# Kernel tuning notes

Hardware: AMD Instinct MI355X
Metric: run time of the kernel (lower is better)

The kernel has to match this reference:

```python
import math
import jax, jax.numpy as jnp
import numpy as np

D_MODEL = 1024
D_CTX = 1024
NUM_HEADS = 16
ATTN_DIM = 1024
HEAD_DIM = ATTN_DIM // NUM_HEADS  # 64
ROPE_GAMMA = 10.0
ROTARY_BASE = 10000.0
ATTN_SCALE = math.sqrt(ATTN_DIM)  # note: module scales by sqrt(attn_dim), not sqrt(head_dim)


def _apply_rope(x, cos, sin):
    # x: [H,B,T,D]; cos/sin: [1,B,T,D//2]
    half = x.shape[-1] // 2
    x1, x2 = x[..., :half], x[..., half:]
    return jnp.concatenate([x1 * cos - x2 * sin, x1 * sin + x2 * cos], axis=-1)


def setup_inputs() -> dict:
    key = jax.random.key(0)
    ks = jax.random.split(key, 12)
    B, T, L = 4, 1024, 1024
    x = jax.random.normal(ks[0], (B, D_MODEL, T), jnp.float32)
    context = jax.random.normal(ks[1], (B, L, D_CTX), jnp.float32)
    # prefix (padding) masks with per-example valid lengths, as in real padded batches
    lens_q = jnp.array([1024, 896, 768, 640])
    lens_k = jnp.array([1024, 960, 832, 704])
    x_mask = (jnp.arange(T)[None, :] < lens_q[:, None]).astype(jnp.int32)[:, None, :]  # [B,1,T]
    context_mask = (jnp.arange(L)[None, :] < lens_k[:, None]).astype(jnp.int32)[:, None, :]  # [B,1,L]
    s = 0.02
    Wq = jax.random.normal(ks[2], (D_MODEL, ATTN_DIM), jnp.float32) * s
    bq = jax.random.normal(ks[3], (ATTN_DIM,), jnp.float32) * s
    Wk = jax.random.normal(ks[4], (D_CTX, ATTN_DIM), jnp.float32) * s
    bk = jax.random.normal(ks[5], (ATTN_DIM,), jnp.float32) * s
    Wv = jax.random.normal(ks[6], (D_CTX, ATTN_DIM), jnp.float32) * s
    bv = jax.random.normal(ks[7], (ATTN_DIM,), jnp.float32) * s
    Wo = jax.random.normal(ks[8], (ATTN_DIM, D_MODEL), jnp.float32) * s
    bo = jax.random.normal(ks[9], (D_MODEL,), jnp.float32) * s
    return {"x": x, "context": context, "x_mask": x_mask, "context_mask": context_mask,
            "Wq": Wq, "bq": bq, "Wk": Wk, "bk": bk, "Wv": Wv, "bv": bv, "Wo": Wo, "bo": bo}


def reference(x, context, x_mask, context_mask, Wq, bq, Wk, bk, Wv, bv, Wo, bo):
    B, _, T = x.shape
    L = context.shape[1]
    H, D = NUM_HEADS, HEAD_DIM
    xm = x_mask.astype(jnp.float32)          # [B,1,T]
    cmf = context_mask.astype(jnp.float32)   # [B,1,L]

    q = jnp.swapaxes(x, 1, 2) @ Wq + bq      # [B,T,attn_dim]
    k = context @ Wk + bk                    # [B,L,attn_dim]
    v = context @ Wv + bv                    # [B,L,attn_dim]

    q = q.reshape(B, T, H, D).transpose(2, 0, 1, 3)  # [H,B,T,D]
    k = k.reshape(B, L, H, D).transpose(2, 0, 1, 3)  # [H,B,L,D]
    v = v.reshape(B, L, H, D).transpose(2, 0, 1, 3)  # [H,B,L,D]

    # length-normalized RoPE (LARoPE)
    len_q = xm.sum(axis=(-2, -1)).reshape(-1, 1, 1)   # [B,1,1]
    len_k = cmf.sum(axis=(-2, -1)).reshape(-1, 1, 1)  # [B,1,1]
    pos_q = jnp.arange(T, dtype=jnp.float32).reshape(1, -1, 1)
    pos_k = jnp.arange(L, dtype=jnp.float32).reshape(1, -1, 1)
    inv_freq = 1.0 / (ROTARY_BASE ** (jnp.arange(0, D, 2, dtype=jnp.float32) / D))
    theta = (inv_freq * ROPE_GAMMA).reshape(1, 1, -1)  # [1,1,D//2]
    freqs_q = (pos_q / len_q) * theta  # [B,T,D//2]
    freqs_k = (pos_k / len_k) * theta  # [B,L,D//2]
    q = _apply_rope(q, jnp.cos(freqs_q)[None], jnp.sin(freqs_q)[None])
    k = _apply_rope(k, jnp.cos(freqs_k)[None], jnp.sin(freqs_k)[None])

    logits = jnp.einsum('hbtd,hbld->hbtl', q, k) / ATTN_SCALE  # [H,B,T,L]
    key_pad = (context_mask == 0)[None]  # [1,B,1,L]
    logits = jnp.where(key_pad, -jnp.inf, logits)
    attn = jax.nn.softmax(logits, axis=-1)
    query_pad = (x_mask == 0).transpose(1, 0, 2)[..., None]  # [1,B,T,1]
    attn = jnp.where(query_pad, 0.0, attn)

    out = jnp.einsum('hbtl,hbld->hbtd', attn, v)          # [H,B,T,D]
    out = out.transpose(1, 2, 0, 3).reshape(B, T, ATTN_DIM)
    out = out @ Wo + bo                                   # [B,T,d_model]
    out = out * jnp.swapaxes(xm, 1, 2)                    # [B,T,1] broadcast
    return jnp.swapaxes(out, 1, 2)                        # [B,d_model,T]
```

## Files before the change

### kernel.cpp

```cpp
#include <hip/hip_runtime.h>
#include <hip/hip_bf16.h>

typedef __attribute__((ext_vector_type(8))) short s8v;
typedef __attribute__((ext_vector_type(4))) float f4v;
typedef __attribute__((ext_vector_type(4))) unsigned short u4v;
typedef __attribute__((ext_vector_type(2))) unsigned int u2v;

#define NH 16

__device__ __forceinline__ unsigned short f2bf(float f) {
  union { float f; unsigned int u; } v; v.f = f;
  unsigned int r = (v.u + 0x7fffu + ((v.u >> 16) & 1u)) >> 16;
  return (unsigned short)r;
}
__device__ __forceinline__ void gll16(const void* g, void* l) {
  __builtin_amdgcn_global_load_lds((const __attribute__((address_space(1))) void*)g,
                                   (__attribute__((address_space(3))) void*)l, 16, 0, 0);
}
__device__ __forceinline__ unsigned int cvtpk(float lo, float hi) {
  unsigned int r;
  asm volatile("v_cvt_pk_bf16_f32 %0, %1, %2" : "=v"(r) : "v"(lo), "v"(hi));
  return r;
}

__global__ __launch_bounds__(256) void prep_kernel(
    const float* __restrict__ x, const float* __restrict__ ctx,
    const float* __restrict__ Wq, const float* __restrict__ Wk,
    const float* __restrict__ Wv, const float* __restrict__ Wo,
    const int* __restrict__ xm, const int* __restrict__ cm,
    unsigned short* __restrict__ xT, unsigned short* __restrict__ ctxb,
    unsigned short* __restrict__ WqT, unsigned short* __restrict__ WkT,
    unsigned short* __restrict__ WvT, unsigned short* __restrict__ WoT,
    float* __restrict__ lens, float2* __restrict__ rope) {
  const int z = blockIdx.z;
  const int tid = threadIdx.x;
  if (z == 12) {
    if (blockIdx.x | blockIdx.y) return;
    const int w = tid >> 6, lane = tid & 63;
    const int g = w * 2 + (lane >> 5);
    const int l32 = lane & 31;
    const int* m = (g < 4) ? (xm + g * 1024) : (cm + (g - 4) * 1024);
    int s = 0;
    for (int i = l32; i < 1024; i += 32) s += m[i];
    for (int o = 16; o; o >>= 1) s += __shfl_xor(s, o);
    if (l32 == 0) lens[g] = (float)s;
    return;
  }
  if (z == 13) {
    const int idx = blockIdx.y * 32 + blockIdx.x;
    if (idx >= 256) return;
    const int which = idx >> 7;
    const int b = (idx >> 5) & 3;
    const int t0 = (idx & 31) * 32;
    const int* m = (which ? cm : xm) + b * 1024;
    const int lane = tid & 63;
    int s = 0;
    for (int i = lane; i < 1024; i += 64) s += m[i];
    for (int o = 32; o; o >>= 1) s += __shfl_xor(s, o);
    const float len = (float)s;
    const int j = tid & 31;
    const float theta = 10.0f * __expf((float)j * -0.28782313662425572f);
    float2* rt = rope + ((size_t)(which * 4 + b) << 15);
    for (int it = 0; it < 4; ++it) {
      const int t = t0 + (tid >> 5) + it * 8;
      const float fr = (float)t / len * theta;
      float sn, cs;
      __sincosf(fr, &sn, &cs);
      rt[t * 32 + j] = make_float2(cs, sn);
    }
    return;
  }
  if (z >= 8) {
    const float* in = ctx + ((size_t)(z - 8) << 20);
    unsigned short* out = ctxb + ((size_t)(z - 8) << 20);
    const int i = (blockIdx.y * 32 + blockIdx.x) * 1024 + tid * 4;
    const f4v v = *(const f4v*)&in[i];
    u4v o;
#pragma unroll
    for (int j = 0; j < 4; ++j) o[j] = f2bf(v[j]);
    *(u4v*)&out[i] = o;
    return;
  }
  __shared__ unsigned short tile[32][33];
  const float* in;
  unsigned short* out;
  if (z < 4)      { in = x + ((size_t)z << 20); out = xT + ((size_t)z << 20); }
  else if (z == 4){ in = Wq; out = WqT; }
  else if (z == 5){ in = Wk; out = WkT; }
  else if (z == 6){ in = Wv; out = WvT; }
  else            { in = Wo; out = WoT; }
  const int r0 = blockIdx.y * 32, c0 = blockIdx.x * 32;
  const int tx = tid & 31, ty = tid >> 5;
  for (int i = ty; i < 32; i += 8) tile[i][tx] = f2bf(in[(size_t)(r0 + i) * 1024 + c0 + tx]);
  __syncthreads();
  for (int i = ty; i < 32; i += 8) out[(size_t)(c0 + i) * 1024 + r0 + tx] = tile[tx][i];
}

#define STAGE_QKV(buf, kt_) do {                                         \
    const int kn_ = (kt_) * 64;                                          \
    _Pragma("unroll")                                                    \
    for (int i_ = 0; i_ < 4; ++i_) {                                     \
      gll16(Ap + i_ * 32 * 1024 + kn_, &As[buf][(i_ * 256 + tid) * 8]);  \
      gll16(Bp + i_ * 32 * 1024 + kn_, &Bs[buf][(i_ * 256 + tid) * 8]);  \
    }                                                                    \
  } while (0)

__global__ __launch_bounds__(256) void gemm_qkv_kernel(
    const unsigned short* __restrict__ xT, const unsigned short* __restrict__ ctxb,
    const unsigned short* __restrict__ WqT, const unsigned short* __restrict__ WkT,
    const unsigned short* __restrict__ WvT,
    const float* __restrict__ bq, const float* __restrict__ bk, const float* __restrict__ bv,
    unsigned short* __restrict__ Qb, unsigned short* __restrict__ Kb,
    unsigned short* __restrict__ Vtb, const float2* __restrict__ rope) {
  __shared__ __attribute__((aligned(16))) unsigned short As[2][8192];
  __shared__ __attribute__((aligned(16))) unsigned short Bs[2][8192];
  const int id = blockIdx.x + (blockIdx.y << 3) + (blockIdx.z << 8);
  const int rest = id >> 3;
  const int my = (id & 7) + ((rest & 3) << 3);
  const int nx = (rest >> 2) & 7;
  const int mode = rest >> 5;
  const unsigned short* A  = (mode == 0) ? xT : ctxb;
  const unsigned short* Bt = (mode == 0) ? WqT : (mode == 1) ? WkT : WvT;
  const float* bias        = (mode == 0) ? bq : (mode == 1) ? bk : bv;
  const int tid = threadIdx.x;
  const int lane = tid & 63, w = tid >> 6;
  const int lq = lane & 15, lg = lane >> 4;
  const int m0 = my * 128, n0 = nx * 128;
  const int wm = (w & 1) * 64, wn = (w >> 1) * 64;
  const int cswz = (lq & 7) << 3;
  const int srow = tid >> 3;
  const int scol = ((tid & 7) * 8) ^ ((srow & 7) << 3);
  const unsigned short* Ap = A + (size_t)(m0 + srow) * 1024 + scol;
  const unsigned short* Bp = Bt + (size_t)(n0 + srow) * 1024 + scol;
  f4v acc[4][4] = {};

  STAGE_QKV(0, 0);
  STAGE_QKV(1, 1);

  for (int kt = 0; kt < 16; ++kt) {
    const int cur = kt & 1;
    if (kt < 15) {
      asm volatile("s_waitcnt vmcnt(8)" ::: "memory");
    } else {
      asm volatile("s_waitcnt vmcnt(0)" ::: "memory");
    }
    __builtin_amdgcn_s_barrier();
#pragma unroll
    for (int kc = 0; kc < 2; ++kc) {
      s8v af[4], bfr[4];
#pragma unroll
      for (int i = 0; i < 4; ++i)
        af[i] = *(const s8v*)&As[cur][(wm + i * 16 + lq) * 64 + ((kc * 32 + lg * 8) ^ cswz)];
#pragma unroll
      for (int i = 0; i < 4; ++i)
        bfr[i] = *(const s8v*)&Bs[cur][(wn + i * 16 + lq) * 64 + ((kc * 32 + lg * 8) ^ cswz)];
#pragma unroll
      for (int mi = 0; mi < 4; ++mi)
#pragma unroll
        for (int ni = 0; ni < 4; ++ni)
          acc[mi][ni] = __builtin_amdgcn_mfma_f32_16x16x32_bf16(af[mi], bfr[ni], acc[mi][ni], 0, 0, 0);
    }
    __builtin_amdgcn_s_barrier();
    if (kt + 2 < 16) STAGE_QKV(cur, kt + 2);
  }

  float bv4[4];
#pragma unroll
  for (int ni = 0; ni < 4; ++ni) bv4[ni] = bias[n0 + wn + ni * 16 + lq];
  const int b = m0 >> 10;

  if (mode <= 1) {
    unsigned short* O = mode ? Kb : Qb;
    const float2* rt = rope + ((size_t)(mode * 4 + b) << 15);
    const int h = (n0 + wn) >> 6;
#pragma unroll
    for (int mi = 0; mi < 4; ++mi) {
#pragma unroll
      for (int rr = 0; rr < 4; ++rr) {
        const int m = m0 + wm + mi * 16 + lg * 4 + rr;
        const int t = m & 1023;
#pragma unroll
        for (int ni = 0; ni < 2; ++ni) {
          const int jj = ni * 16 + lq;
          const float2 cs2 = rt[t * 32 + jj];
          const float x1 = acc[mi][ni][rr] + bv4[ni];
          const float x2 = acc[mi][ni + 2][rr] + bv4[ni + 2];
          unsigned short* bp = &O[((size_t)((b * NH + h) * 1024 + t)) * 64 + jj];
          bp[0] = f2bf(x1 * cs2.x - x2 * cs2.y);
          bp[32] = f2bf(x1 * cs2.y + x2 * cs2.x);
        }
      }
    }
  } else {
#pragma unroll
    for (int mi = 0; mi < 4; ++mi) {
      const int mbase = m0 + wm + mi * 16 + lg * 4;
      const int l0 = mbase & 1023;
#pragma unroll
      for (int ni = 0; ni < 4; ++ni) {
        const int n = n0 + wn + ni * 16 + lq;
        const int hh = n >> 6, d = n & 63;
        u4v pk;
#pragma unroll
        for (int rr = 0; rr < 4; ++rr) pk[rr] = f2bf(acc[mi][ni][rr] + bv4[ni]);
        *(u4v*)&Vtb[((size_t)((b * NH + hh) * 64 + d)) * 1024 + l0] = pk;
      }
    }
  }
}

__global__ __launch_bounds__(256) void gemm_o_kernel(
    const unsigned short* __restrict__ A, const unsigned short* __restrict__ Bt,
    const float* __restrict__ bias, float* __restrict__ Cout,
    const int* __restrict__ xmask) {
  __shared__ __attribute__((aligned(16))) unsigned short As[2][8192];
  __shared__ __attribute__((aligned(16))) unsigned short Bs[2][8192];
  const int id = blockIdx.x + (blockIdx.y << 3);
  const int rest = id >> 3;
  const int my = (id & 7) + ((rest & 3) << 3);
  const int nx = rest >> 2;
  const int tid = threadIdx.x;
  const int lane = tid & 63, w = tid >> 6;
  const int lq = lane & 15, lg = lane >> 4;
  const int m0 = my * 128, n0 = nx * 128;
  const int wm = (w & 1) * 64, wn = (w >> 1) * 64;
  const int cswz = (lq & 7) << 3;
  const int srow = tid >> 3;
  const int scol = ((tid & 7) * 8) ^ ((srow & 7) << 3);
  const unsigned short* Ap = A + (size_t)(m0 + srow) * 1024 + scol;
  const unsigned short* Bp = Bt + (size_t)(n0 + srow) * 1024 + scol;
  f4v acc[4][4] = {};

  STAGE_QKV(0, 0);
  STAGE_QKV(1, 1);

  for (int kt = 0; kt < 16; ++kt) {
    const int cur = kt & 1;
    if (kt < 15) {
      asm volatile("s_waitcnt vmcnt(8)" ::: "memory");
    } else {
      asm volatile("s_waitcnt vmcnt(0)" ::: "memory");
    }
    __builtin_amdgcn_s_barrier();
#pragma unroll
    for (int kc = 0; kc < 2; ++kc) {
      s8v af[4], bfr[4];
#pragma unroll
      for (int i = 0; i < 4; ++i)
        af[i] = *(const s8v*)&As[cur][(wm + i * 16 + lq) * 64 + ((kc * 32 + lg * 8) ^ cswz)];
#pragma unroll
      for (int i = 0; i < 4; ++i)
        bfr[i] = *(const s8v*)&Bs[cur][(wn + i * 16 + lq) * 64 + ((kc * 32 + lg * 8) ^ cswz)];
#pragma unroll
      for (int mi = 0; mi < 4; ++mi)
#pragma unroll
        for (int ni = 0; ni < 4; ++ni)
          acc[mi][ni] = __builtin_amdgcn_mfma_f32_16x16x32_bf16(af[mi], bfr[ni], acc[mi][ni], 0, 0, 0);
    }
    __builtin_amdgcn_s_barrier();
    if (kt + 2 < 16) STAGE_QKV(cur, kt + 2);
  }

  float bv4[4];
#pragma unroll
  for (int ni = 0; ni < 4; ++ni) bv4[ni] = bias[n0 + wn + ni * 16 + lq];
  const int b = m0 >> 10;
#pragma unroll
  for (int mi = 0; mi < 4; ++mi) {
    const int mbase = m0 + wm + mi * 16 + lg * 4;
    const int t0 = mbase & 1023;
#pragma unroll
    for (int ni = 0; ni < 4; ++ni) {
      const int n = n0 + wn + ni * 16 + lq;
      f4v pk;
#pragma unroll
      for (int rr = 0; rr < 4; ++rr) {
        float v = acc[mi][ni][rr] + bv4[ni];
        v *= (float)xmask[b * 1024 + t0 + rr];
        pk[rr] = v;
      }
      *(f4v*)&Cout[(size_t)b * 1024 * 1024 + (size_t)n * 1024 + t0] = pk;
    }
  }
}

__global__ __launch_bounds__(512) void attn_kernel(
    const unsigned short* __restrict__ Q, const unsigned short* __restrict__ K,
    const unsigned short* __restrict__ Vt, const float* __restrict__ lens,
    unsigned short* __restrict__ Aout) {
  __shared__ __attribute__((aligned(16))) unsigned short Ks[2][4096];
  __shared__ __attribute__((aligned(16))) unsigned short Vs[2][4096];
  __shared__ __attribute__((aligned(16))) unsigned short Plds[8][16][72];
  const int tid = threadIdx.x;
  const int lane = tid & 63, w = tid >> 6;
  const int lq = lane & 15, lg = lane >> 4;
  const int id = blockIdx.x + (blockIdx.y << 3);
  const int bh = (id & 7) + (((id >> 3) & 7) << 3);
  const int qblk = id >> 6;
  const int b = bh >> 4, h = bh & 15;
  const int lenq = (int)lens[b];
  if (qblk * 128 >= lenq) return;
  const int lenk = (int)lens[4 + b];
  const int nkt = (lenk + 63) >> 6;
  const int qrow = qblk * 128 + w * 16;
  const unsigned short* Qp = Q + ((size_t)bh * 1024 + qrow) * 64;
  const unsigned short* Kp = K + (size_t)bh * 65536;
  const unsigned short* Vp = Vt + (size_t)bh * 65536;
  const s8v qf0 = *(const s8v*)&Qp[lq * 64 + lg * 8];
  const s8v qf1 = *(const s8v*)&Qp[lq * 64 + 32 + lg * 8];
  const int r0 = tid >> 3;
  const int c0x = ((tid & 7) * 8) ^ ((r0 & 7) << 3);
  const int cswz = (lq & 7) << 3;

  gll16(&Kp[(size_t)r0 * 64 + c0x], &Ks[0][tid * 8]);
  gll16(&Vp[(size_t)r0 * 1024 + c0x], &Vs[0][tid * 8]);
  __syncthreads();

  const float SC2 = 0.0450842200277f;
  float m_run = -1e30f, s_run = 0.0f;
  f4v ot[4] = {};
  for (int kt = 0; kt < nkt; ++kt) {
    const int p = kt & 1;
    if (kt + 1 < nkt) {
      const int kn = (kt + 1) * 64;
      gll16(&Kp[(size_t)(kn + r0) * 64 + c0x], &Ks[p ^ 1][tid * 8]);
      gll16(&Vp[(size_t)r0 * 1024 + kn + c0x], &Vs[p ^ 1][tid * 8]);
    }
    const int k0 = kt * 64;
    const bool full = (k0 + 64 <= lenk);
    float pvv[16];
    float tmax = -1e30f;
    __builtin_amdgcn_s_setprio(1);
#pragma unroll
    for (int kk = 0; kk < 4; ++kk) {
      const int krow = kk * 16 + lq;
      const s8v a0 = *(const s8v*)&Ks[p][krow * 64 + ((lg * 8) ^ cswz)];
      const s8v a1 = *(const s8v*)&Ks[p][krow * 64 + ((32 + lg * 8) ^ cswz)];
      f4v s = {};
      s = __builtin_amdgcn_mfma_f32_16x16x32_bf16(a0, qf0, s, 0, 0, 0);
      s = __builtin_amdgcn_mfma_f32_16x16x32_bf16(a1, qf1, s, 0, 0, 0);
#pragma unroll
      for (int rr = 0; rr < 4; ++rr) {
        float v = s[rr] * SC2;
        if (!full) {
          const int key = k0 + kk * 16 + lg * 4 + rr;
          if (key >= lenk) v = -1e30f;
        }
        pvv[kk * 4 + rr] = v;
        tmax = fmaxf(tmax, v);
      }
    }
    __builtin_amdgcn_s_setprio(0);
    tmax = fmaxf(tmax, __shfl_xor(tmax, 16));
    tmax = fmaxf(tmax, __shfl_xor(tmax, 32));
    if (__any(tmax > m_run + 8.0f)) {
      const float m_new = fmaxf(m_run, tmax);
      const float alpha = exp2f(m_run - m_new);
#pragma unroll
      for (int d = 0; d < 4; ++d)
#pragma unroll
        for (int j = 0; j < 4; ++j) ot[d][j] *= alpha;
      s_run *= alpha;
      m_run = m_new;
    }
    float psum = 0.0f;
#pragma unroll
    for (int kk = 0; kk < 4; ++kk) {
      const float e0 = exp2f(pvv[kk * 4 + 0] - m_run);
      const float e1 = exp2f(pvv[kk * 4 + 1] - m_run);
      const float e2 = exp2f(pvv[kk * 4 + 2] - m_run);
      const float e3 = exp2f(pvv[kk * 4 + 3] - m_run);
      psum += (e0 + e1) + (e2 + e3);
      u2v pw;
      pw[0] = cvtpk(e0, e1);
      pw[1] = cvtpk(e2, e3);
      *(u2v*)&Plds[w][lq][kk * 16 + lg * 4] = pw;
    }
    psum += __shfl_xor(psum, 16);
    psum += __shfl_xor(psum, 32);
    s_run += psum;
    const s8v pb0 = *(const s8v*)&Plds[w][lq][lg * 8];
    const s8v pb1 = *(const s8v*)&Plds[w][lq][32 + lg * 8];
    __builtin_amdgcn_s_setprio(1);
#pragma unroll
    for (int d = 0; d < 4; ++d) {
      const int vrow = d * 16 + lq;
      const s8v av0 = *(const s8v*)&Vs[p][vrow * 64 + ((lg * 8) ^ cswz)];
      const s8v av1 = *(const s8v*)&Vs[p][vrow * 64 + ((32 + lg * 8) ^ cswz)];
      ot[d] = __builtin_amdgcn_mfma_f32_16x16x32_bf16(av0, pb0, ot[d], 0, 0, 0);
      ot[d] = __builtin_amdgcn_mfma_f32_16x16x32_bf16(av1, pb1, ot[d], 0, 0, 0);
    }
    __builtin_amdgcn_s_setprio(0);
    if (kt + 1 < nkt) __syncthreads();
  }
  const float inv = 1.0f / s_run;
  const int t = qrow + lq;
  unsigned short* op = Aout + ((size_t)(b * 1024 + t)) * 1024 + h * 64;
#pragma unroll
  for (int d = 0; d < 4; ++d) {
    u4v oo;
#pragma unroll
    for (int rr = 0; rr < 4; ++rr) oo[rr] = f2bf(ot[d][rr] * inv);
    *(u4v*)&op[d * 16 + lg * 4] = oo;
  }
}

extern "C" void kernel_launch(void* const* d_in, const int* in_sizes, int n_in,
                              void* d_out, int out_size, void* d_ws, size_t ws_size,
                              hipStream_t stream) {
  const float* x   = (const float*)d_in[0];
  const float* ctx = (const float*)d_in[1];
  const int* xm = (const int*)d_in[2];
  const int* cm = (const int*)d_in[3];
  const float* Wq = (const float*)d_in[4];
  const float* bq = (const float*)d_in[5];
  const float* Wk = (const float*)d_in[6];
  const float* bk = (const float*)d_in[7];
  const float* Wv = (const float*)d_in[8];
  const float* bv = (const float*)d_in[9];
  const float* Wo = (const float*)d_in[10];
  const float* bo = (const float*)d_in[11];

  char* ws = (char*)d_ws;
  const size_t MB = 1024 * 1024;
  unsigned short* xT   = (unsigned short*)(ws);
  unsigned short* AOb  = (unsigned short*)(ws);
  unsigned short* ctxb = (unsigned short*)(ws + 8 * MB);
  unsigned short* WqT  = (unsigned short*)(ws + 16 * MB);
  unsigned short* WkT  = (unsigned short*)(ws + 18 * MB);
  unsigned short* WvT  = (unsigned short*)(ws + 20 * MB);
  unsigned short* WoT  = (unsigned short*)(ws + 22 * MB);
  unsigned short* Qb   = (unsigned short*)(ws + 24 * MB);
  unsigned short* Kb   = (unsigned short*)(ws + 32 * MB);
  unsigned short* Vtb  = (unsigned short*)(ws + 40 * MB);
  float* lens          = (float*)(ws + 48 * MB);
  float2* rope         = (float2*)(ws + 49 * MB);

  prep_kernel<<<dim3(32, 32, 14), 256, 0, stream>>>(x, ctx, Wq, Wk, Wv, Wo, xm, cm,
                                                    xT, ctxb, WqT, WkT, WvT, WoT, lens, rope);
  gemm_qkv_kernel<<<dim3(8, 32, 3), 256, 0, stream>>>(xT, ctxb, WqT, WkT, WvT,
                                                      bq, bk, bv, Qb, Kb, Vtb, rope);
  attn_kernel<<<dim3(8, 64), 512, 0, stream>>>(Qb, Kb, Vtb, lens, AOb);
  gemm_o_kernel<<<dim3(8, 32), 256, 0, stream>>>(AOb, WoT, bo, (float*)d_out, xm);
}
```

Measured before the change: 115.1 us.

## Split attention over two key halves and merge partials in a combine kernel

Splits each attention block's key range into two halves of 512, doubling the grid so more workgroups run concurrently. Each half writes a normalized bf16 partial output plus its running max and sum, and a new combine kernel merges the two halves into the final attention output. The softmax scale is also folded into Q in the QKV GEMM epilogue, which removes a multiply per logit. The cost is an extra kernel launch, round-tripping the partial outputs through the output buffer, and an extra bf16 rounding of the partials.

Measured after the change: 123.4 us. 7.2% more time.

```diff
diff --git a/kernel.cpp b/kernel.cpp
--- a/kernel.cpp
+++ b/kernel.cpp
@@ -12,6 +12,10 @@
   union { float f; unsigned int u; } v; v.f = f;
   unsigned int r = (v.u + 0x7fffu + ((v.u >> 16) & 1u)) >> 16;
   return (unsigned short)r;
+}
+__device__ __forceinline__ float bf2f(unsigned short u) {
+  union { unsigned int u; float f; } v; v.u = ((unsigned int)u) << 16;
+  return v.f;
 }
 __device__ __forceinline__ void gll16(const void* g, void* l) {
   __builtin_amdgcn_global_load_lds((const __attribute__((address_space(1))) void*)g,
@@ -171,6 +175,7 @@
 
   if (mode <= 1) {
     unsigned short* O = mode ? Kb : Qb;
+    const float osc = mode ? 1.0f : 0.0450842200277f;
     const float2* rt = rope + ((size_t)(mode * 4 + b) << 15);
     const int h = (n0 + wn) >> 6;
 #pragma unroll
@@ -186,8 +191,8 @@
           const float x1 = acc[mi][ni][rr] + bv4[ni];
           const float x2 = acc[mi][ni + 2][rr] + bv4[ni + 2];
           unsigned short* bp = &O[((size_t)((b * NH + h) * 1024 + t)) * 64 + jj];
-          bp[0] = f2bf(x1 * cs2.x - x2 * cs2.y);
-          bp[32] = f2bf(x1 * cs2.y + x2 * cs2.x);
+          bp[0] = f2bf((x1 * cs2.x - x2 * cs2.y) * osc);
+          bp[32] = f2bf((x1 * cs2.y + x2 * cs2.x) * osc);
         }
       }
     }
@@ -287,25 +292,29 @@
 __global__ __launch_bounds__(512) void attn_kernel(
     const unsigned short* __restrict__ Q, const unsigned short* __restrict__ K,
     const unsigned short* __restrict__ Vt, const float* __restrict__ lens,
-    unsigned short* __restrict__ Aout) {
+    unsigned short* __restrict__ Opart, float2* __restrict__ msbuf) {
   __shared__ __attribute__((aligned(16))) unsigned short Ks[2][4096];
   __shared__ __attribute__((aligned(16))) unsigned short Vs[2][4096];
   __shared__ __attribute__((aligned(16))) unsigned short Plds[8][16][72];
   const int tid = threadIdx.x;
   const int lane = tid & 63, w = tid >> 6;
   const int lq = lane & 15, lg = lane >> 4;
-  const int id = blockIdx.x + (blockIdx.y << 3);
-  const int bh = (id & 7) + (((id >> 3) & 7) << 3);
-  const int qblk = id >> 6;
+  const int id = blockIdx.x + (blockIdx.y << 4);
+  const int bh = id & 63;
+  const int rest = id >> 6;
+  const int qblk = rest & 7;
+  const int half = rest >> 3;
   const int b = bh >> 4, h = bh & 15;
   const int lenq = (int)lens[b];
   if (qblk * 128 >= lenq) return;
   const int lenk = (int)lens[4 + b];
-  const int nkt = (lenk + 63) >> 6;
+  const int kstart = half << 9;
+  const int kend = min(lenk, kstart + 512);
+  const int nkt = (kend - kstart + 63) >> 6;
   const int qrow = qblk * 128 + w * 16;
   const unsigned short* Qp = Q + ((size_t)bh * 1024 + qrow) * 64;
-  const unsigned short* Kp = K + (size_t)bh * 65536;
-  const unsigned short* Vp = Vt + (size_t)bh * 65536;
+  const unsigned short* Kp = K + (size_t)bh * 65536 + (size_t)kstart * 64;
+  const unsigned short* Vp = Vt + (size_t)bh * 65536 + kstart;
   const s8v qf0 = *(const s8v*)&Qp[lq * 64 + lg * 8];
   const s8v qf1 = *(const s8v*)&Qp[lq * 64 + 32 + lg * 8];
   const int r0 = tid >> 3;
@@ -316,7 +325,6 @@
   gll16(&Vp[(size_t)r0 * 1024 + c0x], &Vs[0][tid * 8]);
   __syncthreads();
 
-  const float SC2 = 0.0450842200277f;
   float m_run = -1e30f, s_run = 0.0f;
   f4v ot[4] = {};
   for (int kt = 0; kt < nkt; ++kt) {
@@ -326,8 +334,8 @@
       gll16(&Kp[(size_t)(kn + r0) * 64 + c0x], &Ks[p ^ 1][tid * 8]);
       gll16(&Vp[(size_t)r0 * 1024 + kn + c0x], &Vs[p ^ 1][tid * 8]);
     }
-    const int k0 = kt * 64;
-    const bool full = (k0 + 64 <= lenk);
+    const int k0 = kstart + kt * 64;
+    const bool full = (k0 + 64 <= kend);
     float pvv[16];
     float tmax = -1e30f;
     __builtin_amdgcn_s_setprio(1);
@@ -341,10 +349,10 @@
       s = __builtin_amdgcn_mfma_f32_16x16x32_bf16(a1, qf1, s, 0, 0, 0);
 #pragma unroll
       for (int rr = 0; rr < 4; ++rr) {
-        float v = s[rr] * SC2;
+        float v = s[rr];
         if (!full) {
           const int key = k0 + kk * 16 + lg * 4 + rr;
-          if (key >= lenk) v = -1e30f;
+          if (key >= kend) v = -1e30f;
         }
         pvv[kk * 4 + rr] = v;
         tmax = fmaxf(tmax, v);
@@ -395,7 +403,7 @@
   }
   const float inv = 1.0f / s_run;
   const int t = qrow + lq;
-  unsigned short* op = Aout + ((size_t)(b * 1024 + t)) * 1024 + h * 64;
+  unsigned short* op = Opart + (size_t)half * 4194304 + ((size_t)(b * 1024 + t)) * 1024 + h * 64;
 #pragma unroll
   for (int d = 0; d < 4; ++d) {
     u4v oo;
@@ -403,6 +411,37 @@
     for (int rr = 0; rr < 4; ++rr) oo[rr] = f2bf(ot[d][rr] * inv);
     *(u4v*)&op[d * 16 + lg * 4] = oo;
   }
+  if (lg == 0) msbuf[(size_t)(half * 64 + bh) * 1024 + t] = make_float2(m_run, s_run);
+}
+
+__global__ __launch_bounds__(256) void combine_kernel(
+    const unsigned short* __restrict__ Opart, const float2* __restrict__ msbuf,
+    const float* __restrict__ lens, unsigned short* __restrict__ AOb) {
+  const int tid = threadIdx.x;
+  const int row = blockIdx.x * 2 + (tid >> 7);
+  const int b = row >> 10, t = row & 1023;
+  if (t >= (int)lens[b]) return;
+  const int c8 = (tid & 127) * 8;
+  const int h = c8 >> 6;
+  const int bh = b * 16 + h;
+  const float2 ms0 = msbuf[(size_t)bh * 1024 + t];
+  const float2 ms1 = msbuf[(size_t)(64 + bh) * 1024 + t];
+  const float M = fmaxf(ms0.x, ms1.x);
+  const float w0 = ms0.y * exp2f(ms0.x - M);
+  const float w1 = ms1.y * exp2f(ms1.x - M);
+  const float inv = 1.0f / (w0 + w1);
+  const float a0 = w0 * inv, a1 = w1 * inv;
+  const size_t off = (size_t)row * 1024 + c8;
+  const s8v o0 = *(const s8v*)&Opart[off];
+  const s8v o1 = *(const s8v*)&Opart[4194304 + off];
+  u4v r0, r1;
+#pragma unroll
+  for (int j = 0; j < 4; ++j) {
+    r0[j] = f2bf(bf2f((unsigned short)o0[j]) * a0 + bf2f((unsigned short)o1[j]) * a1);
+    r1[j] = f2bf(bf2f((unsigned short)o0[j + 4]) * a0 + bf2f((unsigned short)o1[j + 4]) * a1);
+  }
+  *(u4v*)&AOb[off] = r0;
+  *(u4v*)&AOb[off + 4] = r1;
 }
 
 extern "C" void kernel_launch(void* const* d_in, const int* in_sizes, int n_in,
@@ -435,11 +474,14 @@
   unsigned short* Vtb  = (unsigned short*)(ws + 40 * MB);
   float* lens          = (float*)(ws + 48 * MB);
   float2* rope         = (float2*)(ws + 49 * MB);
+  float2* msbuf        = (float2*)(ws + 51 * MB);
+  unsigned short* Opart = (unsigned short*)d_out;
 
   prep_kernel<<<dim3(32, 32, 14), 256, 0, stream>>>(x, ctx, Wq, Wk, Wv, Wo, xm, cm,
                                                     xT, ctxb, WqT, WkT, WvT, WoT, lens, rope);
   gemm_qkv_kernel<<<dim3(8, 32, 3), 256, 0, stream>>>(xT, ctxb, WqT, WkT, WvT,
                                                       bq, bk, bv, Qb, Kb, Vtb, rope);
-  attn_kernel<<<dim3(8, 64), 512, 0, stream>>>(Qb, Kb, Vtb, lens, AOb);
+  attn_kernel<<<dim3(16, 64), 512, 0, stream>>>(Qb, Kb, Vtb, lens, Opart, msbuf);
+  combine_kernel<<<2048, 256, 0, stream>>>(Opart, msbuf, lens, AOb);
   gemm_o_kernel<<<dim3(8, 32), 256, 0, stream>>>(AOb, WoT, bo, (float*)d_out, xm);
 }
```

## Skip padded row tiles in QKV and output GEMMs; fold softmax scale into Q

Applied to the files above, without the earlier changes.

The QKV GEMM now returns early for 128-row tiles lying entirely beyond the per-batch valid length. The output GEMM writes zeros for such tiles and skips the matmul. The attention softmax scale (log2e/sqrt(attn_dim)) is folded into Q at the projection epilogue, removing a multiply per logit. Skipped Q/K/V rows are left uninitialized in the workspace, so correctness depends on attention never reading K/V past lenk or Q rows past lenq. Scaling Q before the bf16 rounding also changes rounding slightly.

Measured after the change: 116.9 us. About the same (+1.6%).

```diff
diff --git a/kernel.cpp b/kernel.cpp
--- a/kernel.cpp
+++ b/kernel.cpp
@@ -111,7 +111,8 @@
     const unsigned short* __restrict__ WvT,
     const float* __restrict__ bq, const float* __restrict__ bk, const float* __restrict__ bv,
     unsigned short* __restrict__ Qb, unsigned short* __restrict__ Kb,
-    unsigned short* __restrict__ Vtb, const float2* __restrict__ rope) {
+    unsigned short* __restrict__ Vtb, const float2* __restrict__ rope,
+    const float* __restrict__ lens) {
   __shared__ __attribute__((aligned(16))) unsigned short As[2][8192];
   __shared__ __attribute__((aligned(16))) unsigned short Bs[2][8192];
   const int id = blockIdx.x + (blockIdx.y << 3) + (blockIdx.z << 8);
@@ -119,6 +120,9 @@
   const int my = (id & 7) + ((rest & 3) << 3);
   const int nx = (rest >> 2) & 7;
   const int mode = rest >> 5;
+  const int b = my >> 3;
+  const int lim = (int)lens[(mode == 0 ? 0 : 4) + b];
+  if (((my & 7) << 7) >= lim) return;
   const unsigned short* A  = (mode == 0) ? xT : ctxb;
   const unsigned short* Bt = (mode == 0) ? WqT : (mode == 1) ? WkT : WvT;
   const float* bias        = (mode == 0) ? bq : (mode == 1) ? bk : bv;
@@ -167,10 +171,10 @@
   float bv4[4];
 #pragma unroll
   for (int ni = 0; ni < 4; ++ni) bv4[ni] = bias[n0 + wn + ni * 16 + lq];
-  const int b = m0 >> 10;
 
   if (mode <= 1) {
     unsigned short* O = mode ? Kb : Qb;
+    const float osc = mode ? 1.0f : 0.0450842200277f;
     const float2* rt = rope + ((size_t)(mode * 4 + b) << 15);
     const int h = (n0 + wn) >> 6;
 #pragma unroll
@@ -186,8 +190,8 @@
           const float x1 = acc[mi][ni][rr] + bv4[ni];
           const float x2 = acc[mi][ni + 2][rr] + bv4[ni + 2];
           unsigned short* bp = &O[((size_t)((b * NH + h) * 1024 + t)) * 64 + jj];
-          bp[0] = f2bf(x1 * cs2.x - x2 * cs2.y);
-          bp[32] = f2bf(x1 * cs2.y + x2 * cs2.x);
+          bp[0] = f2bf((x1 * cs2.x - x2 * cs2.y) * osc);
+          bp[32] = f2bf((x1 * cs2.y + x2 * cs2.x) * osc);
         }
       }
     }
@@ -212,7 +216,7 @@
 __global__ __launch_bounds__(256) void gemm_o_kernel(
     const unsigned short* __restrict__ A, const unsigned short* __restrict__ Bt,
     const float* __restrict__ bias, float* __restrict__ Cout,
-    const int* __restrict__ xmask) {
+    const int* __restrict__ xmask, const float* __restrict__ lens) {
   __shared__ __attribute__((aligned(16))) unsigned short As[2][8192];
   __shared__ __attribute__((aligned(16))) unsigned short Bs[2][8192];
   const int id = blockIdx.x + (blockIdx.y << 3);
@@ -224,6 +228,22 @@
   const int lq = lane & 15, lg = lane >> 4;
   const int m0 = my * 128, n0 = nx * 128;
   const int wm = (w & 1) * 64, wn = (w >> 1) * 64;
+  const int b = my >> 3;
+
+  if (((my & 7) << 7) >= (int)lens[b]) {
+#pragma unroll
+    for (int mi = 0; mi < 4; ++mi) {
+      const int t0 = (m0 + wm + mi * 16 + lg * 4) & 1023;
+      const f4v z = {};
+#pragma unroll
+      for (int ni = 0; ni < 4; ++ni) {
+        const int n = n0 + wn + ni * 16 + lq;
+        *(f4v*)&Cout[(size_t)b * 1024 * 1024 + (size_t)n * 1024 + t0] = z;
+      }
+    }
+    return;
+  }
+
   const int cswz = (lq & 7) << 3;
   const int srow = tid >> 3;
   const int scol = ((tid & 7) * 8) ^ ((srow & 7) << 3);
@@ -264,7 +284,6 @@
   float bv4[4];
 #pragma unroll
   for (int ni = 0; ni < 4; ++ni) bv4[ni] = bias[n0 + wn + ni * 16 + lq];
-  const int b = m0 >> 10;
 #pragma unroll
   for (int mi = 0; mi < 4; ++mi) {
     const int mbase = m0 + wm + mi * 16 + lg * 4;
@@ -316,7 +335,6 @@
   gll16(&Vp[(size_t)r0 * 1024 + c0x], &Vs[0][tid * 8]);
   __syncthreads();
 
-  const float SC2 = 0.0450842200277f;
   float m_run = -1e30f, s_run = 0.0f;
   f4v ot[4] = {};
   for (int kt = 0; kt < nkt; ++kt) {
@@ -341,7 +359,7 @@
       s = __builtin_amdgcn_mfma_f32_16x16x32_bf16(a1, qf1, s, 0, 0, 0);
 #pragma unroll
       for (int rr = 0; rr < 4; ++rr) {
-        float v = s[rr] * SC2;
+        float v = s[rr];
         if (!full) {
           const int key = k0 + kk * 16 + lg * 4 + rr;
           if (key >= lenk) v = -1e30f;
@@ -439,7 +457,7 @@
   prep_kernel<<<dim3(32, 32, 14), 256, 0, stream>>>(x, ctx, Wq, Wk, Wv, Wo, xm, cm,
                                                     xT, ctxb, WqT, WkT, WvT, WoT, lens, rope);
   gemm_qkv_kernel<<<dim3(8, 32, 3), 256, 0, stream>>>(xT, ctxb, WqT, WkT, WvT,
-                                                      bq, bk, bv, Qb, Kb, Vtb, rope);
+                                                      bq, bk, bv, Qb, Kb, Vtb, rope, lens);
   attn_kernel<<<dim3(8, 64), 512, 0, stream>>>(Qb, Kb, Vtb, lens, AOb);
-  gemm_o_kernel<<<dim3(8, 32), 256, 0, stream>>>(AOb, WoT, bo, (float*)d_out, xm);
-}
+  gemm_o_kernel<<<dim3(8, 32), 256, 0, stream>>>(AOb, WoT, bo, (float*)d_out, xm, lens);
+}
```
